# Kernel tuning notes

Hardware: AMD Instinct MI355X
Metric: run time of the kernel (lower is better)

## Reference

```python
import jax, jax.numpy as jnp
import numpy as np

HEADS = 16
D_MODEL = 1024
HEAD_DIM = D_MODEL // HEADS


def setup_inputs() -> dict:
    key = jax.random.key(0)
    ks = jax.random.split(key, 11)
    B, S, D = 2, 2048, D_MODEL
    s = 1.0 / np.sqrt(D)
    inp = {
        'Q': jax.random.normal(ks[0], (B, S, D), jnp.float32),
        'K': jax.random.normal(ks[1], (B, S, D), jnp.float32),
        'V': jax.random.normal(ks[2], (B, S, D), jnp.float32),
        'Wq': jax.random.normal(ks[3], (D, D), jnp.float32) * s,
        'Wk': jax.random.normal(ks[4], (D, D), jnp.float32) * s,
        'Wv': jax.random.normal(ks[5], (D, D), jnp.float32) * s,
        'Wo': jax.random.normal(ks[6], (D, D), jnp.float32) * s,
        'bq': jnp.zeros((D,), jnp.float32),
        'bk': jnp.zeros((D,), jnp.float32),
        'bv': jnp.zeros((D,), jnp.float32),
        'bo': jnp.zeros((D,), jnp.float32),
    }
    return inp


def reference(Q, K, V, Wq, Wk, Wv, Wo, bq, bk, bv, bo):
    B, S, D = Q.shape
    H, Dh = HEADS, HEAD_DIM
    # projections (torch Linear: x @ W.T + b)
    q = (Q @ Wq.T + bq).reshape(B, S, H, Dh).transpose(0, 2, 1, 3)  # [B,H,S,Dh]
    k = (K @ Wk.T + bk).reshape(B, S, H, Dh).transpose(0, 2, 1, 3)
    v = (V @ Wv.T + bv).reshape(B, S, H, Dh).transpose(0, 2, 1, 3)
    # naive scaled dot-product attention, scale = 1/sqrt(head_dim)
    scores = jnp.einsum('bhqd,bhkd->bhqk', q, k) / jnp.sqrt(jnp.float32(Dh))
    attn = jax.nn.softmax(scores, axis=-1)
    out = jnp.einsum('bhqk,bhkd->bhqd', attn, v)
    concat = out.transpose(0, 2, 1, 3).reshape(B, S, D)
    return concat @ Wo.T + bo
```

## Files before the change

### kernel.cpp

```cpp
#include <hip/hip_runtime.h>
#include <hip/hip_bf16.h>


#define SEQ     2048
#define DMODEL  1024
#define NHEADS  16
#define DH      64
#define MROWS   4096
#define M1      (1024*1024)
#define M4      (4*1024*1024)
#define SCQ     0.18033688f

typedef __hip_bfloat16 bf16;
typedef __attribute__((ext_vector_type(8))) short  short8;
typedef __attribute__((ext_vector_type(4))) float  f32x4;

__device__ __forceinline__ bf16 f2b(float x) { return __float2bfloat16(x); }
__device__ __forceinline__ f32x4 mfma16(short8 a, short8 b, f32x4 c) {
    return __builtin_amdgcn_mfma_f32_16x16x32_bf16(a, b, c, 0, 0, 0);
}
__device__ __forceinline__ unsigned pk2(float a, float b) {
    union { __hip_bfloat162 h; unsigned u; } x;
    x.h = __float22bfloat162_rn(float2{a, b});
    return x.u;
}
__device__ __forceinline__ short8 pk8(float4 a, float4 b) {
    union { short8 s; unsigned u[4]; } x;
    x.u[0] = pk2(a.x, a.y); x.u[1] = pk2(a.z, a.w);
    x.u[2] = pk2(b.x, b.y); x.u[3] = pk2(b.z, b.w);
    return x.s;
}
__device__ __forceinline__ float fexp2(float x) {
    return __builtin_amdgcn_exp2f(x);
}
#define GLDS(g, l) __builtin_amdgcn_global_load_lds( \
    (const __attribute__((address_space(1))) void*)(g), \
    (__attribute__((address_space(3))) void*)(l), 16, 0, 0)

__global__ __launch_bounds__(256) void cvt_all(
    const float* __restrict__ Wq, const float* __restrict__ Wk,
    const float* __restrict__ Wv, const float* __restrict__ Wo,
    const float* __restrict__ Q,  const float* __restrict__ K,
    const float* __restrict__ V,  bf16* __restrict__ dst)
{
    const size_t gid = (size_t)blockIdx.x * 256 + threadIdx.x;
    const size_t e0 = gid * 8;
    const float* s;
    if (e0 < (size_t)4 * M1) {
        const float* w[4] = {Wq, Wk, Wv, Wo};
        s = w[e0 >> 20] + (e0 & (M1 - 1));
    } else {
        const float* a[4] = {nullptr, Q, K, V};
        s = a[e0 >> 22] + (e0 & (M4 - 1));
    }
    float4 x = *(const float4*)s, y = *(const float4*)(s + 4);
    *(short8*)((short*)dst + e0) = pk8(x, y);
}

__global__ __launch_bounds__(256) void cvt_w(
    const float* __restrict__ W0, const float* __restrict__ W1,
    const float* __restrict__ W2, const float* __restrict__ W3,
    bf16* __restrict__ dst)
{
    const int gid = blockIdx.x * 256 + threadIdx.x;
    const int t   = gid >> 17;
    const int off = (gid & 131071) * 8;
    const float* srcs[4] = {W0, W1, W2, W3};
    const float* s = srcs[t] + off;
    float4 a = *(const float4*)s, b = *(const float4*)(s + 4);
    *(short8*)((short*)dst + (size_t)gid * 8) = pk8(a, b);
}

__global__ __launch_bounds__(256) void cvt_1(
    const float* __restrict__ X, bf16* __restrict__ D)
{
    const int gid = blockIdx.x * 256 + threadIdx.x;
    const int off = gid * 8;
    float4 a = *(const float4*)(X + off), b = *(const float4*)(X + off + 4);
    *(short8*)((short*)D + off) = pk8(a, b);
}

template <int BN>
__device__ __forceinline__ void gemm_body(
    const bf16* __restrict__ A, const bf16* __restrict__ B,
    const float* __restrict__ bias, void* __restrict__ outp,
    int m0, int n0, int mode, int bias_m, float scale)
{
    __shared__ short As[128 * 32];
    __shared__ short Bs[BN * 32];
    constexpr int NI = BN / 32;

    const int tid  = threadIdx.x;
    const int lane = tid & 63;
    const int wv   = tid >> 6;
    const int wm   = (wv >> 1) * 64;
    const int wn   = (wv & 1) * (BN / 2);
    const int fn   = lane & 15;
    const int fq   = lane >> 4;

    const int srow = lane >> 2;
    const int scol = (lane & 3) * 8;

    const short* Ag = (const short*)A;
    const short* Bg = (const short*)B;

    f32x4 acc[4][NI];
#pragma unroll
    for (int i = 0; i < 4; ++i)
#pragma unroll
        for (int j = 0; j < NI; ++j) acc[i][j] = (f32x4){0.f, 0.f, 0.f, 0.f};

    for (int k0 = 0; k0 < DMODEL; k0 += 32) {
#pragma unroll
        for (int i = 0; i < 2; ++i) {
            const int rr = wv * 32 + i * 16;
            const short* ga = Ag + (size_t)(m0 + rr + srow) * DMODEL + k0 + scol;
            GLDS(ga, As + rr * 32);
        }
#pragma unroll
        for (int i = 0; i < BN / 64; ++i) {
            const int rr = wv * (BN / 4) + i * 16;
            const short* gb = Bg + (size_t)(n0 + rr + srow) * DMODEL + k0 + scol;
            GLDS(gb, Bs + rr * 32);
        }
        __syncthreads();

        short8 af[4], bfr[NI];
#pragma unroll
        for (int im = 0; im < 4; ++im)
            af[im] = *(const short8*)(As + (wm + im * 16 + fn) * 32 + fq * 8);
#pragma unroll
        for (int in = 0; in < NI; ++in)
            bfr[in] = *(const short8*)(Bs + (wn + in * 16 + fn) * 32 + fq * 8);
#pragma unroll
        for (int im = 0; im < 4; ++im)
#pragma unroll
            for (int in = 0; in < NI; ++in)
                acc[im][in] = mfma16(af[im], bfr[in], acc[im][in]);
        __syncthreads();
    }

#pragma unroll
    for (int im = 0; im < 4; ++im) {
#pragma unroll
        for (int in = 0; in < NI; ++in) {
#pragma unroll
            for (int r = 0; r < 4; ++r) {
                const int m = m0 + wm + im * 16 + fq * 4 + r;
                const int n = n0 + wn + in * 16 + fn;
                const float c = (acc[im][in][r] + (bias_m ? bias[m] : bias[n])) * scale;
                if (mode == 0) {
                    ((float*)outp)[(size_t)m * DMODEL + n] = c;
                } else if (mode == 1) {
                    const int b = m >> 11, s = m & (SEQ - 1);
                    const int h = n >> 6,  d = n & (DH - 1);
                    ((bf16*)outp)[(((size_t)(b * NHEADS + h) * SEQ) + s) * DH + d] = f2b(c);
                } else {
                    const int h = m >> 6,  d = m & (DH - 1);
                    const int b = n >> 11, s = n & (SEQ - 1);
                    const int p = s & 31;
                    const int sp = (s & ~31) | ((p & 12) << 1) | ((p & 16) >> 2) | (p & 3);
                    ((bf16*)outp)[(((size_t)(b * NHEADS + h) * DH) + d) * SEQ + sp] = f2b(c);
                }
            }
        }
    }
}

__global__ __launch_bounds__(256, 3) void gemm_one(
    const bf16* A, const bf16* B, const float* bias, void* out,
    int mode, int bias_m, float scale)
{
    gemm_body<128>(A, B, bias, out, blockIdx.x * 128, blockIdx.y * 128,
                   mode, bias_m, scale);
}

__global__ __launch_bounds__(256, 3) void gemm_fin(
    const bf16* A, const bf16* B, const float* bias, void* out)
{
    gemm_body<128>(A, B, bias, out, blockIdx.x * 128, blockIdx.y * 128, 0, 0, 1.f);
}

__global__ __launch_bounds__(256, 3) void gemm_qkv(
    const bf16* Qb, const bf16* Kb, const bf16* Vb, const bf16* Wb,
    const float* bq, const float* bk, const float* bv,
    bf16* qp, bf16* kp, bf16* vp)
{
    const int blk = blockIdx.x;
    const int z = blk >> 8, t = blk & 255;
    if (z == 0)
        gemm_body<128>(Qb, Wb,          bq, qp, (t & 31) * 128, (t >> 5) * 128, 1, 0, SCQ);
    else if (z == 1)
        gemm_body<128>(Kb, Wb + M1,     bk, kp, (t & 31) * 128, (t >> 5) * 128, 1, 0, 1.f);
    else
        gemm_body<128>(Wb + 2 * M1, Vb, bv, vp, (t >> 5) * 128, (t & 31) * 128, 2, 1, 1.f);
}


#define QKG(KTB, G, S0, S1) { \
    const short* kr_ = (KTB) + ((G) * 16 + n) * 64; \
    short8 kf0_ = *(const short8*)(kr_ + off0); \
    short8 kf1_ = *(const short8*)(kr_ + off1); \
    S0 = mfma16(kf0_, qf00, Zv); S0 = mfma16(kf1_, qf01, S0); \
    S1 = mfma16(kf0_, qf10, Zv); S1 = mfma16(kf1_, qf11, S1); }

#define PKP(SA, SB, DST) { \
    union { short8 s8; unsigned u[4]; } bb_; \
    bb_.u[0] = pk2(fexp2(SA[0]), fexp2(SA[1])); \
    bb_.u[1] = pk2(fexp2(SA[2]), fexp2(SA[3])); \
    bb_.u[2] = pk2(fexp2(SB[0]), fexp2(SB[1])); \
    bb_.u[3] = pk2(fexp2(SB[2]), fexp2(SB[3])); \
    DST = bb_.s8; }

#define XPH(T, P00, P01, P10, P11) { \
    const short* KtB_ = Kb0 + ((T) & 1) * 4096; \
    f32x4 sa0_, sa1_, sb0_, sb1_; \
    QKG(KtB_, 0, sa0_, sa1_) \
    QKG(KtB_, 1, sb0_, sb1_) \
    PKP(sa0_, sb0_, P00) \
    PKP(sa1_, sb1_, P01) \
    QKG(KtB_, 2, sa0_, sa1_) \
    QKG(KtB_, 3, sb0_, sb1_) \
    PKP(sa0_, sb0_, P10) \
    PKP(sa1_, sb1_, P11) }

#define PVG(VTB, GD, P00, P01, P10, P11) { \
    const short* vr_ = (VTB) + ((GD) * 16 + n) * 64; \
    short8 vf0_ = *(const short8*)(vr_ + off0); \
    short8 vf1_ = *(const short8*)(vr_ + off1); \
    O[GD][0] = mfma16(vf0_, P00, O[GD][0]); \
    O[GD][0] = mfma16(vf1_, P10, O[GD][0]); \
    O[GD][1] = mfma16(vf0_, P01, O[GD][1]); \
    O[GD][1] = mfma16(vf1_, P11, O[GD][1]); }

#define YPH(T, P00, P01, P10, P11) { \
    const short* VtB_ = Vb0 + ((T) & 1) * 4096; \
    __builtin_amdgcn_s_setprio(1); \
    lc0 = mfma16(onesv, P00, lc0); \
    lc1 = mfma16(onesv, P01, lc1); \
    lc0 = mfma16(onesv, P10, lc0); \
    lc1 = mfma16(onesv, P11, lc1); \
    PVG(VtB_, 0, P00, P01, P10, P11) \
    PVG(VtB_, 1, P00, P01, P10, P11) \
    PVG(VtB_, 2, P00, P01, P10, P11) \
    PVG(VtB_, 3, P00, P01, P10, P11) \
    __builtin_amdgcn_s_setprio(0); }

__global__ __launch_bounds__(512, 4) void attn_fused(
    const bf16* __restrict__ q,
    const bf16* __restrict__ k,
    const bf16* __restrict__ vt,
    bf16* __restrict__ out)
{
    __shared__ short LB[32768];

    const int tid  = threadIdx.x;
    const int wave = tid >> 6;
    const int half = wave >> 2;
    const int w4   = wave & 3;
    const int lane = tid & 63;
    const int n    = lane & 15;
    const int quad = lane >> 4;

    const int blk  = blockIdx.x;
    const int xcd  = blk & 7;
    const int rest = blk >> 3;
    const int qt   = rest & 15;
    const int bh   = ((rest >> 4) << 3) | xcd;
    const int q0w  = qt * 128 + w4 * 32;
    const int kt0  = half * 16;

    const bf16* qhead = q  + (size_t)bh * SEQ * DH;
    const bf16* khead = k  + (size_t)bh * SEQ * DH;
    const bf16* vhead = vt + (size_t)bh * DH * SEQ;

    short* Kb0 = LB + half * 16384;
    short* Vb0 = LB + half * 16384 + 8192;

    short8 qf00, qf01, qf10, qf11;
    {
        const short* qr0 = (const short*)(qhead + (size_t)(q0w + n) * DH);
        qf00 = *(const short8*)(qr0 + quad * 8);
        qf01 = *(const short8*)(qr0 + 32 + quad * 8);
        const short* qr1 = (const short*)(qhead + (size_t)(q0w + 16 + n) * DH);
        qf10 = *(const short8*)(qr1 + quad * 8);
        qf11 = *(const short8*)(qr1 + 32 + quad * 8);
    }

    const short8 onesv = {(short)0x3F80, (short)0x3F80, (short)0x3F80, (short)0x3F80,
                          (short)0x3F80, (short)0x3F80, (short)0x3F80, (short)0x3F80};
    const f32x4 Zv = (f32x4){0.f, 0.f, 0.f, 0.f};

    f32x4 O[4][2];
#pragma unroll
    for (int gd = 0; gd < 4; ++gd)
#pragma unroll
        for (int qg = 0; qg < 2; ++qg) O[gd][qg] = Zv;
    f32x4 lc0 = Zv, lc1 = Zv;

    const int srow = lane >> 3;
    const int schk = (lane & 7) ^ srow;
    const int off0 = ((quad       ^ (n & 7)) * 8);
    const int off1 = (((4 + quad) ^ (n & 7)) * 8);

    const char* gk0 = (const char*)khead +
        (size_t)(kt0 * 64 + w4 * 16 + srow) * 128 + schk * 16;
    const char* gv0 = (const char*)vhead +
        (size_t)(w4 * 16 + srow) * 4096 + kt0 * 128 + schk * 16;
    short* const ldsK = Kb0 + (w4 * 16) * 64;
    short* const ldsV = Vb0 + (w4 * 16) * 64;

    auto stageK = [&](int buf) {
        GLDS(gk0,        ldsK + buf * 4096);
        GLDS(gk0 + 1024, ldsK + buf * 4096 + 512);
        gk0 += 8192;
    };
    auto stageV = [&](int buf) {
        GLDS(gv0,         ldsV + buf * 4096);
        GLDS(gv0 + 32768, ldsV + buf * 4096 + 512);
        gv0 += 128;
    };

    short8 PA00, PA01, PA10, PA11;
    short8 PB00, PB01, PB10, PB11;

    stageK(0);

    __syncthreads();
    stageK(1);
    stageV(0);
    XPH(0, PA00, PA01, PA10, PA11)

#pragma unroll 1
    for (int t = 1; t < 15; t += 2) {
        __syncthreads();
        stageK((t + 1) & 1);
        stageV(t & 1);
        XPH(t, PB00, PB01, PB10, PB11)
        YPH(t - 1, PA00, PA01, PA10, PA11)
        __syncthreads();
        stageK((t + 2) & 1);
        stageV((t + 1) & 1);
        XPH(t + 1, PA00, PA01, PA10, PA11)
        YPH(t, PB00, PB01, PB10, PB11)
    }
    __syncthreads();
    stageV(1);
    XPH(15, PB00, PB01, PB10, PB11)
    YPH(14, PA00, PA01, PA10, PA11)
    __syncthreads();
    YPH(15, PB00, PB01, PB10, PB11)

    float* scr = (float*)LB + (size_t)(w4 * 64 + lane) * 34;
    const float l0 = lc0[0];
    const float l1 = lc1[0];

    __syncthreads();
    if (half == 1) {
#pragma unroll
        for (int gd = 0; gd < 4; ++gd)
#pragma unroll
            for (int qg = 0; qg < 2; ++qg) {
                *(float2*)(scr + (gd * 2 + qg) * 4)     = float2{O[gd][qg][0], O[gd][qg][1]};
                *(float2*)(scr + (gd * 2 + qg) * 4 + 2) = float2{O[gd][qg][2], O[gd][qg][3]};
            }
        *(float2*)(scr + 32) = float2{l0, l1};
    }
    __syncthreads();
    if (half == 0) {
        const float2 lo = *(const float2*)(scr + 32);
        const float inv0 = 1.0f / (l0 + lo.x);
        const float inv1 = 1.0f / (l1 + lo.y);
        const int b = bh >> 4;
        const int h = bh & (NHEADS - 1);
#pragma unroll
        for (int gd = 0; gd < 4; ++gd) {
#pragma unroll
            for (int qg = 0; qg < 2; ++qg) {
                const float iv = qg ? inv1 : inv0;
                float2 a = *(const float2*)(scr + (gd * 2 + qg) * 4);
                float2 c = *(const float2*)(scr + (gd * 2 + qg) * 4 + 2);
                const int s = q0w + qg * 16 + n;
                uint2 o;
                o.x = pk2((O[gd][qg][0] + a.x) * iv, (O[gd][qg][1] + a.y) * iv);
                o.y = pk2((O[gd][qg][2] + c.x) * iv, (O[gd][qg][3] + c.y) * iv);
                *(uint2*)(out + ((size_t)(b * SEQ + s)) * DMODEL + h * DH + gd * 16 + quad * 4) = o;
            }
        }
    }
}

#undef QKG
#undef PKP
#undef XPH
#undef PVG
#undef YPH

__global__ __launch_bounds__(256) void attn_mfma(
    const bf16* __restrict__ q,
    const bf16* __restrict__ k,
    const bf16* __restrict__ vt,
    bf16* __restrict__ out)
{
    __shared__ short Kt[2][64 * 64];
    __shared__ short Vt[2][64 * 64];

    const int tid  = threadIdx.x;
    const int wave = tid >> 6;
    const int lane = tid & 63;
    const int n    = lane & 15;
    const int quad = lane >> 4;

    const int blk  = blockIdx.x;
    const int xcd  = blk & 7;
    const int rest = blk >> 3;
    const int qt   = rest & 15;
    const int bh   = ((rest >> 4) << 3) | xcd;
    const int q0w  = qt * 128 + wave * 32;

    const bf16* qhead = q  + (size_t)bh * SEQ * DH;
    const bf16* khead = k  + (size_t)bh * SEQ * DH;
    const bf16* vhead = vt + (size_t)bh * DH * SEQ;

    short8 qf[2][2];
#pragma unroll
    for (int qg = 0; qg < 2; ++qg) {
        const short* qr = (const short*)(qhead + (size_t)(q0w + qg * 16 + n) * DH);
        qf[qg][0] = *(const short8*)(qr + quad * 8);
        qf[qg][1] = *(const short8*)(qr + 32 + quad * 8);
    }

    const short8 onesv = {(short)0x3F80, (short)0x3F80, (short)0x3F80, (short)0x3F80,
                          (short)0x3F80, (short)0x3F80, (short)0x3F80, (short)0x3F80};
    const f32x4 Zv = (f32x4){0.f, 0.f, 0.f, 0.f};

    f32x4 O[4][2];
#pragma unroll
    for (int gd = 0; gd < 4; ++gd)
#pragma unroll
        for (int qg = 0; qg < 2; ++qg) O[gd][qg] = Zv;
    f32x4 lacc[2] = {Zv, Zv};

    const int srow = lane >> 3;
    const int schk = (lane & 7) ^ srow;
    const int off0 = ((quad       ^ (n & 7)) * 8);
    const int off1 = (((4 + quad) ^ (n & 7)) * 8);

    auto stage = [&](int kt, int buf) {
        const int kbase = kt * 64;
#pragma unroll
        for (int i = 0; i < 2; ++i) {
            const int r = wave * 16 + i * 8 + srow;
            const char* gk = (const char*)(khead + (size_t)(kbase + r) * DH) + schk * 16;
            const char* gv = (const char*)(vhead + (size_t)r * SEQ + kbase) + schk * 16;
            GLDS(gk, Kt[buf] + (wave * 16 + i * 8) * 64);
            GLDS(gv, Vt[buf] + (wave * 16 + i * 8) * 64);
        }
    };

    auto tile_body = [&](const short* KtB, const short* VtB) {
        f32x4 st[4][2];
#pragma unroll
        for (int g = 0; g < 4; ++g) {
            const short* kr = KtB + (g * 16 + n) * 64;
            short8 kf0 = *(const short8*)(kr + off0);
            short8 kf1 = *(const short8*)(kr + off1);
#pragma unroll
            for (int qg = 0; qg < 2; ++qg) {
                f32x4 s = mfma16(kf0, qf[qg][0], Zv);
                s = mfma16(kf1, qf[qg][1], s);
                st[g][qg] = s;
            }
        }
        short8 bP[2][2];
#pragma unroll
        for (int t = 0; t < 2; ++t) {
#pragma unroll
            for (int qg = 0; qg < 2; ++qg) {
                union { short8 s8; unsigned u[4]; } bb;
                bb.u[0] = pk2(fexp2(st[2*t][qg][0]),   fexp2(st[2*t][qg][1]));
                bb.u[1] = pk2(fexp2(st[2*t][qg][2]),   fexp2(st[2*t][qg][3]));
                bb.u[2] = pk2(fexp2(st[2*t+1][qg][0]), fexp2(st[2*t+1][qg][1]));
                bb.u[3] = pk2(fexp2(st[2*t+1][qg][2]), fexp2(st[2*t+1][qg][3]));
                bP[t][qg] = bb.s8;
                lacc[qg] = mfma16(onesv, bP[t][qg], lacc[qg]);
            }
        }
#pragma unroll
        for (int gd = 0; gd < 4; ++gd) {
            const short* vr = VtB + (gd * 16 + n) * 64;
            short8 vf0 = *(const short8*)(vr + off0);
            short8 vf1 = *(const short8*)(vr + off1);
#pragma unroll
            for (int qg = 0; qg < 2; ++qg) {
                O[gd][qg] = mfma16(vf0, bP[0][qg], O[gd][qg]);
                O[gd][qg] = mfma16(vf1, bP[1][qg], O[gd][qg]);
            }
        }
    };

    stage(0, 0);
#pragma unroll 1
    for (int kt = 0; kt < SEQ / 64; kt += 2) {
        __syncthreads();
        stage(kt + 1, 1);
        tile_body(Kt[0], Vt[0]);
        __syncthreads();
        if (kt + 2 < SEQ / 64) stage(kt + 2, 0);
        tile_body(Kt[1], Vt[1]);
    }

    const float inv0 = 1.0f / lacc[0][0];
    const float inv1 = 1.0f / lacc[1][0];
    const int b = bh >> 4;
    const int h = bh & (NHEADS - 1);
#pragma unroll
    for (int gd = 0; gd < 4; ++gd) {
#pragma unroll
        for (int qg = 0; qg < 2; ++qg) {
            const float iv = qg ? inv1 : inv0;
            const int s = q0w + qg * 16 + n;
            uint2 o;
            o.x = pk2(O[gd][qg][0] * iv, O[gd][qg][1] * iv);
            o.y = pk2(O[gd][qg][2] * iv, O[gd][qg][3] * iv);
            *(uint2*)(out + ((size_t)(b * SEQ + s)) * DMODEL + h * DH + gd * 16 + quad * 4) = o;
        }
    }
}

extern "C" void kernel_launch(void* const* d_in, const int* in_sizes, int n_in,
                              void* d_out, int out_size, void* d_ws, size_t ws_size,
                              hipStream_t stream) {
    const float* Q  = (const float*)d_in[0];
    const float* K  = (const float*)d_in[1];
    const float* V  = (const float*)d_in[2];
    const float* Wq = (const float*)d_in[3];
    const float* Wk = (const float*)d_in[4];
    const float* Wv = (const float*)d_in[5];
    const float* Wo = (const float*)d_in[6];
    const float* bq = (const float*)d_in[7];
    const float* bk = (const float*)d_in[8];
    const float* bv = (const float*)d_in[9];
    const float* bo = (const float*)d_in[10];

    bf16* kp = (bf16*)d_out;
    bf16* vp = kp + M4;

    dim3 bb(256);
    dim3 gqk(MROWS / 128, DMODEL / 128);
    dim3 gvv(DMODEL / 128, MROWS / 128);
    dim3 gfin(MROWS / 128, DMODEL / 128);

    if (ws_size >= (size_t)40 * 1024 * 1024) {
        bf16* Wb = (bf16*)d_ws;
        bf16* Qb = Wb + 4 * M1;
        bf16* Kb = Qb + M4;
        bf16* Vb = Kb + M4;
        bf16* qp = Vb + M4;
        bf16* ao = Qb;

        cvt_all<<<8192, bb, 0, stream>>>(Wq, Wk, Wv, Wo, Q, K, V, Wb);
        gemm_qkv<<<768, bb, 0, stream>>>(Qb, Kb, Vb, Wb, bq, bk, bv, qp, kp, vp);
        attn_fused<<<512, 512, 0, stream>>>(qp, kp, vp, ao);
        gemm_fin<<<gfin, bb, 0, stream>>>(ao, Wb + 3 * M1, bo, d_out);
    } else {
        bf16* Wb = (bf16*)d_ws;
        bf16* Xb = Wb + 4 * M1;
        bf16* qp = Xb + M4;
        bf16* ao = Xb;

        cvt_w<<<2048, bb, 0, stream>>>(Wq, Wk, Wv, Wo, Wb);
        cvt_1<<<2048, bb, 0, stream>>>(Q, Xb);
        gemm_one<<<gqk, bb, 0, stream>>>(Xb, Wb, bq, qp, 1, 0, SCQ);
        cvt_1<<<2048, bb, 0, stream>>>(K, Xb);
        gemm_one<<<gqk, bb, 0, stream>>>(Xb, Wb + M1, bk, kp, 1, 0, 1.f);
        cvt_1<<<2048, bb, 0, stream>>>(V, Xb);
        gemm_one<<<gvv, bb, 0, stream>>>(Wb + 2 * M1, Xb, bv, vp, 2, 1, 1.f);
        attn_mfma<<<512, bb, 0, stream>>>(qp, kp, vp, ao);
        gemm_fin<<<gfin, bb, 0, stream>>>(ao, Wb + 3 * M1, bo, d_out);
    }
}
```

Before: 209.4 us.

## Load V fragments directly from global and drop V LDS staging

Instead of staging V^T tiles through LDS with async global-to-LDS copies, each wave now reads its V fragments straight from global memory into registers at the start of every key tile. The two-stage software pipeline (XPH of tile t+1 overlapped with YPH of tile t) is collapsed into a simple per-tile loop, and LDS shrinks to roughly half. The aim is to cut LDS traffic and footprint, which may raise occupancy. In exchange, V global reads are repeated by every wave with less latency hiding, and the QK/PV overlap across tiles is lost.

```diff
diff --git a/kernel.cpp b/kernel.cpp
--- a/kernel.cpp
+++ b/kernel.cpp
@@ -224,27 +224,11 @@
     PKP(sa0_, sb0_, P10) \
     PKP(sa1_, sb1_, P11) }
 
-#define PVG(VTB, GD, P00, P01, P10, P11) { \
-    const short* vr_ = (VTB) + ((GD) * 16 + n) * 64; \
-    short8 vf0_ = *(const short8*)(vr_ + off0); \
-    short8 vf1_ = *(const short8*)(vr_ + off1); \
-    O[GD][0] = mfma16(vf0_, P00, O[GD][0]); \
-    O[GD][0] = mfma16(vf1_, P10, O[GD][0]); \
-    O[GD][1] = mfma16(vf0_, P01, O[GD][1]); \
-    O[GD][1] = mfma16(vf1_, P11, O[GD][1]); }
-
-#define YPH(T, P00, P01, P10, P11) { \
-    const short* VtB_ = Vb0 + ((T) & 1) * 4096; \
-    __builtin_amdgcn_s_setprio(1); \
-    lc0 = mfma16(onesv, P00, lc0); \
-    lc1 = mfma16(onesv, P01, lc1); \
-    lc0 = mfma16(onesv, P10, lc0); \
-    lc1 = mfma16(onesv, P11, lc1); \
-    PVG(VtB_, 0, P00, P01, P10, P11) \
-    PVG(VtB_, 1, P00, P01, P10, P11) \
-    PVG(VtB_, 2, P00, P01, P10, P11) \
-    PVG(VtB_, 3, P00, P01, P10, P11) \
-    __builtin_amdgcn_s_setprio(0); }
+#define PVR(GD, VF0, VF1) { \
+    O[GD][0] = mfma16(VF0, P00, O[GD][0]); \
+    O[GD][0] = mfma16(VF1, P10, O[GD][0]); \
+    O[GD][1] = mfma16(VF0, P01, O[GD][1]); \
+    O[GD][1] = mfma16(VF1, P11, O[GD][1]); }
 
 __global__ __launch_bounds__(512, 4) void attn_fused(
     const bf16* __restrict__ q,
@@ -252,7 +236,7 @@
     const bf16* __restrict__ vt,
     bf16* __restrict__ out)
 {
-    __shared__ short LB[32768];
+    __shared__ short LB[17408];
 
     const int tid  = threadIdx.x;
     const int wave = tid >> 6;
@@ -274,8 +258,7 @@
     const bf16* khead = k  + (size_t)bh * SEQ * DH;
     const bf16* vhead = vt + (size_t)bh * DH * SEQ;
 
-    short* Kb0 = LB + half * 16384;
-    short* Vb0 = LB + half * 16384 + 8192;
+    short* Kb0 = LB + half * 8192;
 
     short8 qf00, qf01, qf10, qf11;
     {
@@ -305,51 +288,45 @@
 
     const char* gk0 = (const char*)khead +
         (size_t)(kt0 * 64 + w4 * 16 + srow) * 128 + schk * 16;
-    const char* gv0 = (const char*)vhead +
-        (size_t)(w4 * 16 + srow) * 4096 + kt0 * 128 + schk * 16;
     short* const ldsK = Kb0 + (w4 * 16) * 64;
-    short* const ldsV = Vb0 + (w4 * 16) * 64;
 
     auto stageK = [&](int buf) {
         GLDS(gk0,        ldsK + buf * 4096);
         GLDS(gk0 + 1024, ldsK + buf * 4096 + 512);
         gk0 += 8192;
     };
-    auto stageV = [&](int buf) {
-        GLDS(gv0,         ldsV + buf * 4096);
-        GLDS(gv0 + 32768, ldsV + buf * 4096 + 512);
-        gv0 += 128;
-    };
-
-    short8 PA00, PA01, PA10, PA11;
-    short8 PB00, PB01, PB10, PB11;
+
+    const char* vb = (const char*)vhead + (size_t)n * 4096 + (size_t)kt0 * 128 + quad * 16;
+
+    short8 P00, P01, P10, P11;
 
     stageK(0);
 
-    __syncthreads();
-    stageK(1);
-    stageV(0);
-    XPH(0, PA00, PA01, PA10, PA11)
-
 #pragma unroll 1
-    for (int t = 1; t < 15; t += 2) {
+    for (int t = 0; t < 16; ++t) {
         __syncthreads();
-        stageK((t + 1) & 1);
-        stageV(t & 1);
-        XPH(t, PB00, PB01, PB10, PB11)
-        YPH(t - 1, PA00, PA01, PA10, PA11)
-        __syncthreads();
-        stageK((t + 2) & 1);
-        stageV((t + 1) & 1);
-        XPH(t + 1, PA00, PA01, PA10, PA11)
-        YPH(t, PB00, PB01, PB10, PB11)
-    }
-    __syncthreads();
-    stageV(1);
-    XPH(15, PB00, PB01, PB10, PB11)
-    YPH(14, PA00, PA01, PA10, PA11)
-    __syncthreads();
-    YPH(15, PB00, PB01, PB10, PB11)
+        short8 VA0 = *(const short8*)(vb);
+        short8 VB0 = *(const short8*)(vb + 64);
+        short8 VA1 = *(const short8*)(vb + 65536);
+        short8 VB1 = *(const short8*)(vb + 65536 + 64);
+        short8 VA2 = *(const short8*)(vb + 131072);
+        short8 VB2 = *(const short8*)(vb + 131072 + 64);
+        short8 VA3 = *(const short8*)(vb + 196608);
+        short8 VB3 = *(const short8*)(vb + 196608 + 64);
+        if (t < 15) stageK((t + 1) & 1);
+        XPH(t, P00, P01, P10, P11)
+        __builtin_amdgcn_s_setprio(1);
+        lc0 = mfma16(onesv, P00, lc0);
+        lc1 = mfma16(onesv, P01, lc1);
+        lc0 = mfma16(onesv, P10, lc0);
+        lc1 = mfma16(onesv, P11, lc1);
+        PVR(0, VA0, VB0)
+        PVR(1, VA1, VB1)
+        PVR(2, VA2, VB2)
+        PVR(3, VA3, VB3)
+        __builtin_amdgcn_s_setprio(0);
+        vb += 128;
+    }
 
     float* scr = (float*)LB + (size_t)(w4 * 64 + lane) * 34;
     const float l0 = lc0[0];
@@ -393,8 +370,7 @@
 #undef QKG
 #undef PKP
 #undef XPH
-#undef PVG
-#undef YPH
+#undef PVR
 
 __global__ __launch_bounds__(256) void attn_mfma(
     const bf16* __restrict__ q,
```

New measurement: 258.9 us. +23.7%, slower.
